# Performance work log

Hardware: AMD Instinct MI355X
Metric: run time of the kernel (lower is better)

## Reference

```python
import jax, jax.numpy as jnp
import numpy as np

TEMPERATURE = 0.05   # distiller.temperature
KD_WEIGHT = 1.0      # args.kd_weight
EPS = 1e-8
B, D = 128, 768


def _huber(diff):
    a = jnp.abs(diff)
    return jnp.where(a < 1.0, 0.5 * a * a, a - 0.5)


def _pairwise_sqdist(x):
    # ||xi||^2 + ||xj||^2 - 2 xi.xj  (squared euclidean, as in source)
    n2 = (x * x).sum(axis=1, keepdims=True)
    return n2 + n2.T - 2.0 * (x @ x.T)


def _distance_loss(s, t):
    ds = _pairwise_sqdist(s)          # [N,N]
    dt = _pairwise_sqdist(t)
    n = ds.shape[0]
    mask = jnp.triu(jnp.ones((n, n), bool), k=1)
    cnt = n * (n - 1) / 2.0
    mean_sd = jax.lax.stop_gradient(jnp.where(mask, ds, 0.0).sum() / cnt) + EPS
    mean_td = jnp.where(mask, dt, 0.0).sum() / cnt + EPS  # teacher is constant anyway
    loss = _huber(ds / mean_sd - dt / mean_td)
    return jnp.where(mask, loss, 0.0).sum() / cnt


def _angle_potentials(x):
    # diffs[i,j] = x[j] - x[i]; unit vectors; cos[i,j,k] = e[i,j] . e[k,j]
    diffs = x[None, :, :] - x[:, None, :]                       # [N,N,D]
    e = diffs / (jnp.linalg.norm(diffs, axis=-1, keepdims=True) + EPS)
    return jnp.einsum('ijd,kjd->ijk', e, e)                     # [N,N,N]


def _angle_loss(s, t):
    ps = _angle_potentials(s)
    pt = _angle_potentials(t)
    n = ps.shape[0]
    i = jnp.arange(n)
    # valid iff i != j, i != k, j != k  (matches the three masked diagonals)
    m = ((i[:, None, None] != i[None, :, None]) &
         (i[:, None, None] != i[None, None, :]) &
         (i[None, :, None] != i[None, None, :]))
    cnt = n * (n - 1) * (n - 2)
    return jnp.where(m, _huber(ps - pt), 0.0).sum() / cnt


def _contrastive_loss(sq, sp):
    scores = (sq @ sp.T) / TEMPERATURE                          # [B,B]
    tgt = jnp.arange(scores.shape[0])                           # * (B//B) == arange
    logZ = jax.nn.logsumexp(scores, axis=-1)
    return (logZ - jnp.take_along_axis(scores, tgt[:, None], axis=1)[:, 0]).mean()


def setup_inputs() -> dict:
    key = jax.random.key(0)
    k1, k2, k3, k4 = jax.random.split(key, 4)
    return {
        'student_qry': jax.random.normal(k1, (B, D), jnp.float32),
        'student_pos': jax.random.normal(k2, (B, D), jnp.float32),
        'teacher_qry': jax.random.normal(k3, (B, D), jnp.float32),
        'teacher_pos': jax.random.normal(k4, (B, D), jnp.float32),
    }


def reference(student_qry, student_pos, teacher_qry, teacher_pos):
    contrastive = _contrastive_loss(student_qry, student_pos)
    s = jnp.concatenate([student_qry, student_pos], axis=0)     # [2B,D]
    t = jnp.concatenate([teacher_qry, teacher_pos], axis=0)
    t = jax.lax.stop_gradient(t)                                # teacher under no_grad
    kd = 0.5 * _distance_loss(s, t) + 0.5 * _angle_loss(s, t)
    total = contrastive + KD_WEIGHT * kd
    return total, contrastive, kd
```

## Files before the change

### kernel.cpp

```cpp
#include <hip/hip_runtime.h>
#include <math.h>

#define N2   256
#define DIM  768
#define EPSF 1e-8f
#define MAGIC 0x5A17F00Du

#define OFF_G     0u
#define OFF_DIAG  131072u
#define OFF_TSUM  131584u
#define OFF_SLOT  131712u
#define OFF_FLAG2 132608u
#define SL_ANG  0
#define SL_DIST 512
#define SL_CON  768

typedef __attribute__((ext_vector_type(8))) short short8;
typedef __attribute__((ext_vector_type(4))) float f32x4;

__device__ inline float wave_reduce_sum(float v) {
    #pragma unroll
    for (int o = 32; o > 0; o >>= 1) v += __shfl_down(v, o, 64);
    return v;
}
__device__ inline float wave_reduce_max(float v) {
    #pragma unroll
    for (int o = 32; o > 0; o >>= 1) v = fmaxf(v, __shfl_down(v, o, 64));
    return v;
}
__device__ inline float block_reduce_sum(float v, volatile float* red) {
    float w = wave_reduce_sum(v);
    __syncthreads();
    if ((threadIdx.x & 63) == 0) red[threadIdx.x >> 6] = w;
    __syncthreads();
    return red[0] + red[1] + red[2] + red[3];
}
__device__ inline const float* rowptr(const float* q, const float* p, int r) {
    return (r < 128) ? (r * DIM + q) : ((r - 128) * DIM + p);
}
__device__ inline unsigned f2bf(float x) {
    union { float f; unsigned u; } v; v.f = x;
    return (v.u + 0x7fffu + ((v.u >> 16) & 1u)) >> 16;
}
__device__ inline void st_agent_f(float* p, float v) {
    __hip_atomic_store(p, v, __ATOMIC_RELAXED, __HIP_MEMORY_SCOPE_AGENT);
}
__device__ inline float ld_agent_f(const float* p) {
    return __hip_atomic_load(p, __ATOMIC_RELAXED, __HIP_MEMORY_SCOPE_AGENT);
}
__device__ inline void st_agent_u(unsigned* p, unsigned v) {
    __hip_atomic_store(p, v, __ATOMIC_RELAXED, __HIP_MEMORY_SCOPE_AGENT);
}
__device__ inline unsigned ld_agent_u(const unsigned* p) {
    return __hip_atomic_load(p, __ATOMIC_RELAXED, __HIP_MEMORY_SCOPE_AGENT);
}

__global__ __launch_bounds__(256) void gemm_kernel(
        const float* __restrict__ sq, const float* __restrict__ sp,
        const float* __restrict__ tq, const float* __restrict__ tp,
        float* __restrict__ ws) {
    const int b = blockIdx.x, t = threadIdx.x;
    const int mat = b & 1, tile = b >> 1;
    const int m0 = (tile >> 3) * 32, n0 = (tile & 7) * 32;
    const float* q = mat ? tq : sq;
    const float* p = mat ? tp : sp;

    __shared__ unsigned short Asb[32][104];
    __shared__ unsigned short Bsb[32][104];
    __shared__ float redg[4];

    const int srow = t >> 3, skq = (t & 7) * 12;
    const float* arow = rowptr(q, p, m0 + srow) + skq;
    const float* brow = rowptr(q, p, n0 + srow) + skq;

    float4 pa[3], pb[3];
    #pragma unroll
    for (int m = 0; m < 3; ++m) {
        pa[m] = *(const float4*)&arow[4 * m];
        pb[m] = *(const float4*)&brow[4 * m];
    }

    const int wave = t >> 6, lane = t & 63;
    const int wm = (wave >> 1) * 16, wn = (wave & 1) * 16;
    const int fr = lane & 15;
    const int fk = (lane >> 4) * 8;
    f32x4 acc = {0.f, 0.f, 0.f, 0.f};

    for (int c = 0; c < 8; ++c) {
        #pragma unroll
        for (int m = 0; m < 3; ++m) {
            uint2 ap, bp;
            ap.x = f2bf(pa[m].x) | (f2bf(pa[m].y) << 16);
            ap.y = f2bf(pa[m].z) | (f2bf(pa[m].w) << 16);
            bp.x = f2bf(pb[m].x) | (f2bf(pb[m].y) << 16);
            bp.y = f2bf(pb[m].z) | (f2bf(pb[m].w) << 16);
            *(uint2*)&Asb[srow][skq + 4 * m] = ap;
            *(uint2*)&Bsb[srow][skq + 4 * m] = bp;
        }
        __syncthreads();
        if (c < 7) {
            const int kb = (c + 1) * 96;
            #pragma unroll
            for (int m = 0; m < 3; ++m) {
                pa[m] = *(const float4*)&arow[kb + 4 * m];
                pb[m] = *(const float4*)&brow[kb + 4 * m];
            }
        }
        #pragma unroll
        for (int kc = 0; kc < 96; kc += 32) {
            const short8 a0 = *(const short8*)&Asb[wm + fr][kc + fk];
            const short8 b0 = *(const short8*)&Bsb[wn + fr][kc + fk];
            acc = __builtin_amdgcn_mfma_f32_16x16x32_bf16(a0, b0, acc, 0, 0, 0);
        }
        __syncthreads();
    }

    float* G = ws + OFF_G + (unsigned)mat * 65536u;
    const int crow0 = (lane >> 4) * 4;
    const int ccol = lane & 15;
    float ts = 0.f;
    #pragma unroll
    for (int reg = 0; reg < 4; ++reg) {
        const int row = m0 + wm + crow0 + reg;
        const int col = n0 + wn + ccol;
        G[row * 256 + col] = acc[reg];
        ts += acc[reg];
    }
    if (m0 == n0 && wm == wn && (lane >> 4) == (ccol >> 2)) {
        ws[OFF_DIAG + (unsigned)(mat * 256 + m0 + wm + ccol)] = acc[ccol & 3];
    }
    const float tsum = block_reduce_sum(ts, redg);
    if (t == 0) ws[OFF_TSUM + (unsigned)(mat * 64 + tile)] = tsum;
}

__global__ __launch_bounds__(256, 4) void mega_kernel(float* __restrict__ ws,
                                                      float* __restrict__ out) {
    const float* Pg = ws + OFF_G;
    const float* Dg = ws + OFF_DIAG;
    __shared__ float sGJ[16][68], sTJ[16][68], sIJ[16][68], sITJ[16][68];
    __shared__ float sGI[32][68], sTI[32][68];
    __shared__ float dgS[256], dgT[256];
    __shared__ float red1[4], red2[4], redS[1];
    const int b = blockIdx.x, t = threadIdx.x;

    if (b < 512) {
        const int k0 = (b & 3) * 64;
        const int j0 = ((b >> 2) & 15) * 16;
        const int i0 = (b >> 6) * 32;
        const int jj = t & 15, ii = t >> 4;
        const int i1 = i0 + ii, i2 = i1 + 16, j = j0 + jj;

        dgS[t] = Dg[t];
        dgT[t] = Dg[256 + t];

        const int r = t >> 4, c4 = (t & 15) * 4;
        const unsigned baseJ = (unsigned)((j0 + r) * 256 + k0 + c4);
        const float4 gjs = *(const float4*)&Pg[baseJ];
        const float4 gjt = *(const float4*)&Pg[65536u + baseJ];

        #pragma unroll
        for (int s2 = 0; s2 < 2; ++s2) {
            const int slot = t + 256 * s2;
            const int ri = slot >> 4, ci = (slot & 15) * 4;
            const unsigned base = (unsigned)((i0 + ri) * 256 + k0 + ci);
            *(float4*)&sGI[ri][ci] = *(const float4*)&Pg[base];
            *(float4*)&sTI[ri][ci] = *(const float4*)&Pg[65536u + base];
        }
        const float g1s = Pg[(unsigned)(i1 * 256 + j)];
        const float g1t = Pg[65536u + (unsigned)(i1 * 256 + j)];
        const float g2s = Pg[(unsigned)(i2 * 256 + j)];
        const float g2t = Pg[65536u + (unsigned)(i2 * 256 + j)];
        __syncthreads();

        {
            const float djs = dgS[j0 + r], djt = dgT[j0 + r];
            float4 ivs, ivt;
            const float* dS = &dgS[k0 + c4];
            const float* dT = &dgT[k0 + c4];
            ivs.x = 1.f / (sqrtf(fmaxf(djs + dS[0] - 2.f * gjs.x, 0.f)) + EPSF);
            ivs.y = 1.f / (sqrtf(fmaxf(djs + dS[1] - 2.f * gjs.y, 0.f)) + EPSF);
            ivs.z = 1.f / (sqrtf(fmaxf(djs + dS[2] - 2.f * gjs.z, 0.f)) + EPSF);
            ivs.w = 1.f / (sqrtf(fmaxf(djs + dS[3] - 2.f * gjs.w, 0.f)) + EPSF);
            ivt.x = 1.f / (sqrtf(fmaxf(djt + dT[0] - 2.f * gjt.x, 0.f)) + EPSF);
            ivt.y = 1.f / (sqrtf(fmaxf(djt + dT[1] - 2.f * gjt.y, 0.f)) + EPSF);
            ivt.z = 1.f / (sqrtf(fmaxf(djt + dT[2] - 2.f * gjt.z, 0.f)) + EPSF);
            ivt.w = 1.f / (sqrtf(fmaxf(djt + dT[3] - 2.f * gjt.w, 0.f)) + EPSF);
            *(float4*)&sGJ[r][c4] = gjs;
            *(float4*)&sTJ[r][c4] = gjt;
            *(float4*)&sIJ[r][c4] = ivs;
            *(float4*)&sITJ[r][c4] = ivt;
        }
        const float Gjj = dgS[j], Tjj = dgT[j];
        const float wis1 = 1.f / (sqrtf(fmaxf(dgS[i1] + Gjj - 2.f * g1s, 0.f)) + EPSF);
        const float wit1 = 1.f / (sqrtf(fmaxf(dgT[i1] + Tjj - 2.f * g1t, 0.f)) + EPSF);
        const float wis2 = 1.f / (sqrtf(fmaxf(dgS[i2] + Gjj - 2.f * g2s, 0.f)) + EPSF);
        const float wit2 = 1.f / (sqrtf(fmaxf(dgT[i2] + Tjj - 2.f * g2t, 0.f)) + EPSF);
        const float as1 = (Gjj - g1s) * wis1;
        const float at1 = (Tjj - g1t) * wit1;
        const float as2 = (Gjj - g2s) * wis2;
        const float at2 = (Tjj - g2t) * wit2;
        __syncthreads();

        float sum1 = 0.f, sum2 = 0.f;
        for (int c = 0; c < 64; c += 4) {
            const float4 gJ  = *(const float4*)&sGJ[jj][c];
            const float4 iJ  = *(const float4*)&sIJ[jj][c];
            const float4 tJ  = *(const float4*)&sTJ[jj][c];
            const float4 itJ = *(const float4*)&sITJ[jj][c];
            const float4 a1 = *(const float4*)&sGI[ii][c];
            const float4 b1 = *(const float4*)&sTI[ii][c];
            const float4 a2 = *(const float4*)&sGI[ii + 16][c];
            const float4 b2 = *(const float4*)&sTI[ii + 16][c];
            const float gJr[4]  = {gJ.x, gJ.y, gJ.z, gJ.w};
            const float iJr[4]  = {iJ.x, iJ.y, iJ.z, iJ.w};
            const float tJr[4]  = {tJ.x, tJ.y, tJ.z, tJ.w};
            const float itJr[4] = {itJ.x, itJ.y, itJ.z, itJ.w};
            const float a1r[4] = {a1.x, a1.y, a1.z, a1.w};
            const float b1r[4] = {b1.x, b1.y, b1.z, b1.w};
            const float a2r[4] = {a2.x, a2.y, a2.z, a2.w};
            const float b2r[4] = {b2.x, b2.y, b2.z, b2.w};
            #pragma unroll
            for (int e = 0; e < 4; ++e) {
                const float ps1 = fmaf(wis1, a1r[e] - gJr[e], as1) * iJr[e];
                const float pt1 = fmaf(wit1, b1r[e] - tJr[e], at1) * itJr[e];
                const float d1 = ps1 - pt1;
                const float ad1 = fabsf(d1);
                const float m1 = fminf(ad1, 1.f);
                sum1 = fmaf(m1, fmaf(-0.5f, m1, ad1), sum1);

                const float ps2 = fmaf(wis2, a2r[e] - gJr[e], as2) * iJr[e];
                const float pt2 = fmaf(wit2, b2r[e] - tJr[e], at2) * itJr[e];
                const float d2 = ps2 - pt2;
                const float ad2 = fabsf(d2);
                const float m2 = fminf(ad2, 1.f);
                sum2 = fmaf(m2, fmaf(-0.5f, m2, ad2), sum2);
            }
        }
        const float v = block_reduce_sum(sum1 + sum2, red1);
        if (t == 0) {
            st_agent_f(ws + OFF_SLOT + SL_ANG + b, v);
            asm volatile("s_waitcnt vmcnt(0)" ::: "memory");
            st_agent_u((unsigned*)(ws + OFF_FLAG2) + b, MAGIC);
        }
    } else if (b < 768) {
        const int i = b - 512, j = t;
        const float gs  = Pg[(unsigned)(i * 256 + j)];
        const float gt  = Pg[65536u + (unsigned)(i * 256 + j)];
        const float djs = Dg[j], djt = Dg[256 + j];
        const float dis = Dg[i], dit = Dg[256 + i];
        const float ds = fmaxf(dis + djs - 2.f * gs, 0.f);
        const float dt = fmaxf(dit + djt - 2.f * gt, 0.f);

        const float tr_s = block_reduce_sum(djs, red1);
        const float tr_t = block_reduce_sum(djt, red1);
        const float tv = (t < 128) ? ws[OFF_TSUM + t] : 0.f;
        const float sum_gs = block_reduce_sum((t < 64) ? tv : 0.f, red1);
        const float sum_gt = block_reduce_sum((t >= 64) ? tv : 0.f, red1);
        const float rs = 1.f / ((256.f * tr_s - sum_gs) / 32640.f + EPSF);
        const float rt = 1.f / ((256.f * tr_t - sum_gt) / 32640.f + EPSF);

        const float dd = ds * rs - dt * rt;
        const float a = fabsf(dd);
        const float m = fminf(a, 1.f);
        const float hv = block_reduce_sum((j > i) ? m * fmaf(-0.5f, m, a) : 0.f, red1);
        if (t == 0) {
            st_agent_f(ws + OFF_SLOT + SL_DIST + i, hv);
            asm volatile("s_waitcnt vmcnt(0)" ::: "memory");
            st_agent_u((unsigned*)(ws + OFF_FLAG2) + b, MAGIC);
        }
    } else {
        const int rrow = b - 768, j = t;
        const float gs = (j >= 128) ? Pg[(unsigned)(rrow * 256 + j)] : 0.f;
        const float s = (j >= 128) ? 20.f * gs : -INFINITY;
        if (j == 128 + rrow) redS[0] = s;
        float mx0 = wave_reduce_max(s);
        __syncthreads();
        if ((t & 63) == 0) red2[t >> 6] = mx0;
        __syncthreads();
        const float mx = fmaxf(fmaxf(red2[0], red2[1]), fmaxf(red2[2], red2[3]));
        const float e = block_reduce_sum((j >= 128) ? expf(s - mx) : 0.f, red1);
        if (t == 0) {
            st_agent_f(ws + OFF_SLOT + SL_CON + rrow, mx + logf(e) - redS[0]);
            asm volatile("s_waitcnt vmcnt(0)" ::: "memory");
            st_agent_u((unsigned*)(ws + OFF_FLAG2) + b, MAGIC);
        }
    }

    if (b == 0) {
        for (int k = t; k < 896; k += 256) {
            while (ld_agent_u((const unsigned*)(ws + OFF_FLAG2) + k) != MAGIC)
                __builtin_amdgcn_s_sleep(4);
        }
        asm volatile("s_waitcnt vmcnt(0)" ::: "memory");
        __builtin_amdgcn_sched_barrier(0);
        __syncthreads();

        float* S = ws + OFF_SLOT;
        const float a_ = block_reduce_sum(ld_agent_f(S + SL_ANG + t) +
                                          ld_agent_f(S + SL_ANG + 256 + t), red1);
        const float d_ = block_reduce_sum(ld_agent_f(S + SL_DIST + t), red1);
        const float c_ = block_reduce_sum((t < 128) ? ld_agent_f(S + SL_CON + t)
                                                    : 0.f, red1);
        if (t == 0) {
            const float contrastive = c_ / 128.f;
            const float dist = d_ / 32640.f;
            const float ang = a_ / 16581120.f;
            const float kd = 0.5f * (dist + ang);
            out[0] = contrastive + kd;
            out[1] = contrastive;
            out[2] = kd;
        }
    }
}

extern "C" void kernel_launch(void* const* d_in, const int* in_sizes, int n_in,
                              void* d_out, int out_size, void* d_ws, size_t ws_size,
                              hipStream_t stream) {
    (void)in_sizes; (void)n_in; (void)out_size; (void)ws_size;
    const float* sq = (const float*)d_in[0];
    const float* sp = (const float*)d_in[1];
    const float* tq = (const float*)d_in[2];
    const float* tp = (const float*)d_in[3];
    float* ws  = (float*)d_ws;
    float* out = (float*)d_out;

    gemm_kernel<<<128, 256, 0, stream>>>(sq, sp, tq, tp, ws);
    mega_kernel<<<896, 256, 0, stream>>>(ws, out);
}
```

Baseline: 76.78 us.

## Exploit i/k symmetry in angle loss to compute only upper-triangular tile pairs

The angle potential is symmetric in i and k, so the angle blocks now cover only the upper-triangular (i-tile, k-tile) pairs with 32x32 tiles, and off-diagonal tiles are weighted by two. This cuts the angle arithmetic and Gram loads roughly in half. The cost is a larger grid with smaller per-block work (more blocks and flag slots) and a small loop to decode the triangular index. Slot and flag offsets are shifted to fit the extra blocks.

```diff
diff --git a/kernel.cpp b/kernel.cpp
--- a/kernel.cpp
+++ b/kernel.cpp
@@ -10,10 +10,12 @@
 #define OFF_DIAG  131072u
 #define OFF_TSUM  131584u
 #define OFF_SLOT  131712u
-#define OFF_FLAG2 132608u
+#define OFF_FLAG2 132672u
 #define SL_ANG  0
-#define SL_DIST 512
-#define SL_CON  768
+#define SL_DIST 576
+#define SL_CON  832
+#define NB_ANG  576
+#define NB_ALL  960
 
 typedef __attribute__((ext_vector_type(8))) short short8;
 typedef __attribute__((ext_vector_type(4))) float f32x4;
@@ -137,35 +139,37 @@
                                                       float* __restrict__ out) {
     const float* Pg = ws + OFF_G;
     const float* Dg = ws + OFF_DIAG;
-    __shared__ float sGJ[16][68], sTJ[16][68], sIJ[16][68], sITJ[16][68];
-    __shared__ float sGI[32][68], sTI[32][68];
+    __shared__ float sGJ[16][36], sTJ[16][36], sIJ[16][36], sITJ[16][36];
+    __shared__ float sGI[32][36], sTI[32][36];
     __shared__ float dgS[256], dgT[256];
     __shared__ float red1[4], red2[4], redS[1];
     const int b = blockIdx.x, t = threadIdx.x;
 
-    if (b < 512) {
-        const int k0 = (b & 3) * 64;
-        const int j0 = ((b >> 2) & 15) * 16;
-        const int i0 = (b >> 6) * 32;
-        const int jj = t & 15, ii = t >> 4;
-        const int i1 = i0 + ii, i2 = i1 + 16, j = j0 + jj;
+    if (b < NB_ANG) {
+        const int pr = b >> 4;
+        const int jt = b & 15;
+        int ti = 0, rem = pr;
+        while (rem >= 8 - ti) { rem -= 8 - ti; ++ti; }
+        const int tk = ti + rem;
+        const int i0 = ti * 32, k0 = tk * 32, j0 = jt * 16;
+        const float wgt = (ti == tk) ? 1.f : 2.f;
+
+        const int jj = t & 15, iw = t >> 4;
+        const int i1 = i0 + iw, i2 = i1 + 16, j = j0 + jj;
 
         dgS[t] = Dg[t];
         dgT[t] = Dg[256 + t];
 
-        const int r = t >> 4, c4 = (t & 15) * 4;
-        const unsigned baseJ = (unsigned)((j0 + r) * 256 + k0 + c4);
-        const float4 gjs = *(const float4*)&Pg[baseJ];
-        const float4 gjt = *(const float4*)&Pg[65536u + baseJ];
-
-        #pragma unroll
-        for (int s2 = 0; s2 < 2; ++s2) {
-            const int slot = t + 256 * s2;
-            const int ri = slot >> 4, ci = (slot & 15) * 4;
-            const unsigned base = (unsigned)((i0 + ri) * 256 + k0 + ci);
-            *(float4*)&sGI[ri][ci] = *(const float4*)&Pg[base];
-            *(float4*)&sTI[ri][ci] = *(const float4*)&Pg[65536u + base];
-        }
+        const int r = t >> 4, c2 = (t & 15) * 2;
+        const unsigned baseJ = (unsigned)((j0 + r) * 256 + k0 + c2);
+        const float2 gjs = *(const float2*)&Pg[baseJ];
+        const float2 gjt = *(const float2*)&Pg[65536u + baseJ];
+
+        const int ri = t >> 3, ci = (t & 7) * 4;
+        const unsigned baseI = (unsigned)((i0 + ri) * 256 + k0 + ci);
+        *(float4*)&sGI[ri][ci] = *(const float4*)&Pg[baseI];
+        *(float4*)&sTI[ri][ci] = *(const float4*)&Pg[65536u + baseI];
+
         const float g1s = Pg[(unsigned)(i1 * 256 + j)];
         const float g1t = Pg[65536u + (unsigned)(i1 * 256 + j)];
         const float g2s = Pg[(unsigned)(i2 * 256 + j)];
@@ -174,21 +178,17 @@
 
         {
             const float djs = dgS[j0 + r], djt = dgT[j0 + r];
-            float4 ivs, ivt;
-            const float* dS = &dgS[k0 + c4];
-            const float* dT = &dgT[k0 + c4];
-            ivs.x = 1.f / (sqrtf(fmaxf(djs + dS[0] - 2.f * gjs.x, 0.f)) + EPSF);
-            ivs.y = 1.f / (sqrtf(fmaxf(djs + dS[1] - 2.f * gjs.y, 0.f)) + EPSF);
-            ivs.z = 1.f / (sqrtf(fmaxf(djs + dS[2] - 2.f * gjs.z, 0.f)) + EPSF);
-            ivs.w = 1.f / (sqrtf(fmaxf(djs + dS[3] - 2.f * gjs.w, 0.f)) + EPSF);
-            ivt.x = 1.f / (sqrtf(fmaxf(djt + dT[0] - 2.f * gjt.x, 0.f)) + EPSF);
-            ivt.y = 1.f / (sqrtf(fmaxf(djt + dT[1] - 2.f * gjt.y, 0.f)) + EPSF);
-            ivt.z = 1.f / (sqrtf(fmaxf(djt + dT[2] - 2.f * gjt.z, 0.f)) + EPSF);
-            ivt.w = 1.f / (sqrtf(fmaxf(djt + dT[3] - 2.f * gjt.w, 0.f)) + EPSF);
-            *(float4*)&sGJ[r][c4] = gjs;
-            *(float4*)&sTJ[r][c4] = gjt;
-            *(float4*)&sIJ[r][c4] = ivs;
-            *(float4*)&sITJ[r][c4] = ivt;
+            const float dk0 = dgS[k0 + c2], dk1 = dgS[k0 + c2 + 1];
+            const float ek0 = dgT[k0 + c2], ek1 = dgT[k0 + c2 + 1];
+            float2 ivs, ivt;
+            ivs.x = 1.f / (sqrtf(fmaxf(djs + dk0 - 2.f * gjs.x, 0.f)) + EPSF);
+            ivs.y = 1.f / (sqrtf(fmaxf(djs + dk1 - 2.f * gjs.y, 0.f)) + EPSF);
+            ivt.x = 1.f / (sqrtf(fmaxf(djt + ek0 - 2.f * gjt.x, 0.f)) + EPSF);
+            ivt.y = 1.f / (sqrtf(fmaxf(djt + ek1 - 2.f * gjt.y, 0.f)) + EPSF);
+            *(float2*)&sGJ[r][c2] = gjs;
+            *(float2*)&sTJ[r][c2] = gjt;
+            *(float2*)&sIJ[r][c2] = ivs;
+            *(float2*)&sITJ[r][c2] = ivt;
         }
         const float Gjj = dgS[j], Tjj = dgT[j];
         const float wis1 = 1.f / (sqrtf(fmaxf(dgS[i1] + Gjj - 2.f * g1s, 0.f)) + EPSF);
@@ -202,15 +202,16 @@
         __syncthreads();
 
         float sum1 = 0.f, sum2 = 0.f;
-        for (int c = 0; c < 64; c += 4) {
+        #pragma unroll
+        for (int c = 0; c < 32; c += 4) {
             const float4 gJ  = *(const float4*)&sGJ[jj][c];
             const float4 iJ  = *(const float4*)&sIJ[jj][c];
             const float4 tJ  = *(const float4*)&sTJ[jj][c];
             const float4 itJ = *(const float4*)&sITJ[jj][c];
-            const float4 a1 = *(const float4*)&sGI[ii][c];
-            const float4 b1 = *(const float4*)&sTI[ii][c];
-            const float4 a2 = *(const float4*)&sGI[ii + 16][c];
-            const float4 b2 = *(const float4*)&sTI[ii + 16][c];
+            const float4 a1 = *(const float4*)&sGI[iw][c];
+            const float4 b1 = *(const float4*)&sTI[iw][c];
+            const float4 a2 = *(const float4*)&sGI[iw + 16][c];
+            const float4 b2 = *(const float4*)&sTI[iw + 16][c];
             const float gJr[4]  = {gJ.x, gJ.y, gJ.z, gJ.w};
             const float iJr[4]  = {iJ.x, iJ.y, iJ.z, iJ.w};
             const float tJr[4]  = {tJ.x, tJ.y, tJ.z, tJ.w};
@@ -238,12 +239,12 @@
         }
         const float v = block_reduce_sum(sum1 + sum2, red1);
         if (t == 0) {
-            st_agent_f(ws + OFF_SLOT + SL_ANG + b, v);
+            st_agent_f(ws + OFF_SLOT + SL_ANG + b, v * wgt);
             asm volatile("s_waitcnt vmcnt(0)" ::: "memory");
             st_agent_u((unsigned*)(ws + OFF_FLAG2) + b, MAGIC);
         }
-    } else if (b < 768) {
-        const int i = b - 512, j = t;
+    } else if (b < NB_ANG + 256) {
+        const int i = b - NB_ANG, j = t;
         const float gs  = Pg[(unsigned)(i * 256 + j)];
         const float gt  = Pg[65536u + (unsigned)(i * 256 + j)];
         const float djs = Dg[j], djt = Dg[256 + j];
@@ -269,7 +270,7 @@
             st_agent_u((unsigned*)(ws + OFF_FLAG2) + b, MAGIC);
         }
     } else {
-        const int rrow = b - 768, j = t;
+        const int rrow = b - (NB_ANG + 256), j = t;
         const float gs = (j >= 128) ? Pg[(unsigned)(rrow * 256 + j)] : 0.f;
         const float s = (j >= 128) ? 20.f * gs : -INFINITY;
         if (j == 128 + rrow) redS[0] = s;
@@ -287,7 +288,7 @@
     }
 
     if (b == 0) {
-        for (int k = t; k < 896; k += 256) {
+        for (int k = t; k < NB_ALL; k += 256) {
             while (ld_agent_u((const unsigned*)(ws + OFF_FLAG2) + k) != MAGIC)
                 __builtin_amdgcn_s_sleep(4);
         }
@@ -296,8 +297,9 @@
         __syncthreads();
 
         float* S = ws + OFF_SLOT;
-        const float a_ = block_reduce_sum(ld_agent_f(S + SL_ANG + t) +
-                                          ld_agent_f(S + SL_ANG + 256 + t), red1);
+        const float a_ = block_reduce_sum(
+            ld_agent_f(S + SL_ANG + t) + ld_agent_f(S + SL_ANG + 256 + t) +
+            ((t < 64) ? ld_agent_f(S + SL_ANG + 512 + t) : 0.f), red1);
         const float d_ = block_reduce_sum(ld_agent_f(S + SL_DIST + t), red1);
         const float c_ = block_reduce_sum((t < 128) ? ld_agent_f(S + SL_CON + t)
                                                     : 0.f, red1);
@@ -325,5 +327,5 @@
     float* out = (float*)d_out;
 
     gemm_kernel<<<128, 256, 0, stream>>>(sq, sp, tq, tp, ws);
-    mega_kernel<<<896, 256, 0, stream>>>(ws, out);
-}
+    mega_kernel<<<NB_ALL, 256, 0, stream>>>(ws, out);
+}
```

Result: no change. 75.37 us (-1.8%).
